# Kernel tuning notes

Measured on AMD Instinct MI355X. Metric: run time of the kernel, lower is better.

The kernel has to match this reference:

```python
import jax, jax.numpy as jnp
import numpy as np

D = 1024
KERNEL = 4

def setup_inputs() -> dict:
    key = jax.random.key(0)
    ks = jax.random.split(key, 8)
    B, L, d = 4, 8192, D
    x = jax.random.normal(ks[0], (B, L, d), dtype=jnp.float32)
    conv_weight = jax.random.normal(ks[1], (d, 1, KERNEL), dtype=jnp.float32) * 0.02
    conv_bias = jnp.zeros((d,), dtype=jnp.float32)
    lim = 1.0 / np.sqrt(d)
    Wr_w = jax.random.uniform(ks[2], (d, d), jnp.float32, -lim, lim)
    Wr_b = jax.random.uniform(ks[3], (d,), jnp.float32, -lim, lim)
    Wi_w = jax.random.uniform(ks[4], (d, d), jnp.float32, -lim, lim)
    Wi_b = jax.random.uniform(ks[5], (d,), jnp.float32, -lim, lim)
    log_a = jnp.full((d,), 7.5, dtype=jnp.float32)
    out_w = jax.random.uniform(ks[6], (d, d), jnp.float32, -lim, lim)
    norm_w = jnp.ones((d,), dtype=jnp.float32)
    return {"x": x, "conv_weight": conv_weight, "conv_bias": conv_bias,
            "Wr_w": Wr_w, "Wr_b": Wr_b, "Wi_w": Wi_w, "Wi_b": Wi_b,
            "log_a": log_a, "out_w": out_w, "norm_w": norm_w}

def _causal_depthwise_conv(x, w, b):
    # x: [B,L,d], w: [d,1,K], b: [d]. out[t] = sum_k w[:,0,k] * x[t-3+k] + b
    B, L, d = x.shape
    xp = jnp.pad(x, ((0, 0), (KERNEL - 1, 0), (0, 0)))
    out = b[None, None, :]
    for k in range(KERNEL):  # small fixed kernel loop
        out = out + xp[:, k:k + L, :] * w[:, 0, k][None, None, :]
    return out

def _parallel_scan(a_t, b_t):
    # h_t = a_t * h_{t-1} + b_t via log-space cumsum; float32 throughout
    a = a_t.astype(jnp.float32)
    b = b_t.astype(jnp.float32)
    log_A = jnp.clip(jnp.cumsum(jnp.log(jnp.clip(a, 1e-7)), axis=1), -80.0, None)
    A = jnp.exp(log_A)
    h = A * jnp.cumsum(b * jnp.exp(-log_A), axis=1)
    return h.astype(a_t.dtype)

def _rmsnorm(x, w, eps=1e-6):
    ms = jnp.mean(jnp.square(x.astype(jnp.float32)), axis=-1, keepdims=True)
    return (x * jax.lax.rsqrt(ms + eps)).astype(x.dtype) * w

def reference(x, conv_weight, conv_bias, Wr_w, Wr_b, Wi_w, Wi_b, log_a, out_w, norm_w):
    x_conv = _causal_depthwise_conv(x, conv_weight, conv_bias)          # [B,L,d]
    r_t = jax.nn.sigmoid(x_conv @ Wr_w.T + Wr_b)
    i_t = jax.nn.sigmoid(x_conv @ Wi_w.T + Wi_b)
    a_base = jax.nn.sigmoid(log_a.astype(jnp.float32)).astype(x.dtype)
    a_t = jnp.power(a_base[None, None, :], 8.0 * r_t)
    b_t = jnp.sqrt(jnp.clip(1.0 - a_t * a_t, 1e-6, None)) * (i_t * x_conv)
    h = _parallel_scan(a_t, b_t)
    return _rmsnorm(h @ out_w.T, norm_w)
```

## Files before the change

### kernel.cpp

```cpp
#include <hip/hip_runtime.h>
#include <hip/hip_bf16.h>

#define D 1024
#define KW 4
#define SEQL 8192
#define BATCH 4
#define MROWS (BATCH*SEQL)
#define SEG 128
#define NSEG (SEQL/SEG)

using bf16 = __hip_bfloat16;
typedef __attribute__((ext_vector_type(8))) short bf16x8_t;
typedef __attribute__((ext_vector_type(4))) float f32x4_t;

__device__ __forceinline__ float sigmoid_f(float x){ return 1.0f/(1.0f + __expf(-x)); }

__device__ __forceinline__ void gload_lds16(const bf16* g, bf16* l){
  __builtin_amdgcn_global_load_lds(
    (const __attribute__((address_space(1))) unsigned int*)g,
    (__attribute__((address_space(3))) unsigned int*)l,
    16, 0, 0);
}

__device__ __forceinline__ void bf16x2_unpack(unsigned int u, float& lo, float& hi){
  union { unsigned int i; float f; } a, b;
  a.i = (u & 0xffffu) << 16;
  b.i = u & 0xffff0000u;
  lo = a.f; hi = b.f;
}
__device__ __forceinline__ unsigned int bf16x2_pack(float lo, float hi){
  unsigned short l = __builtin_bit_cast(unsigned short, __float2bfloat16(lo));
  unsigned short h = __builtin_bit_cast(unsigned short, __float2bfloat16(hi));
  return (unsigned int)l | ((unsigned int)h << 16);
}

__global__ __launch_bounds__(256) void prep_k(const float* __restrict__ Wr, const float* __restrict__ Wi,
                                              const float* __restrict__ Wrb, const float* __restrict__ Wib,
                                              const float* __restrict__ Wo,
                                              bf16* __restrict__ W1, bf16* __restrict__ Wob,
                                              float* __restrict__ b1){
  int idx = blockIdx.x*256 + threadIdx.x;
  if (idx < 2*D*D){
    int n = idx >> 10;
    float v = (n < D) ? Wr[idx] : Wi[idx - D*D];
    W1[idx] = __float2bfloat16(v);
  } else if (idx < 3*D*D){
    int j = idx - 2*D*D;
    Wob[j] = __float2bfloat16(Wo[j]);
  }
  if (idx < 2*D){
    b1[idx] = (idx < D) ? Wrb[idx] : Wib[idx - D];
  }
}

__global__ __launch_bounds__(256) void conv_k(const float* __restrict__ x, const float* __restrict__ w,
                                              const float* __restrict__ bias,
                                              unsigned int* __restrict__ xcb){
  int idx = blockIdx.x*256 + threadIdx.x;
  int c2 = idx & 511;
  int c  = c2 * 2;
  int m  = idx >> 9;
  int l  = m & (SEQL-1);
  const float* wp = w + c*KW;
  float2 b2 = *(const float2*)(bias + c);
  const float* xm = x + (size_t)m*D + c;
  float2 v3 = *(const float2*)xm;
  float2 v2 = (l>=1)? *(const float2*)(xm - D)   : make_float2(0.f,0.f);
  float2 v1 = (l>=2)? *(const float2*)(xm - 2*D) : make_float2(0.f,0.f);
  float2 v0 = (l>=3)? *(const float2*)(xm - 3*D) : make_float2(0.f,0.f);
  float a0 = b2.x + wp[0]*v0.x + wp[1]*v1.x + wp[2]*v2.x + wp[3]*v3.x;
  float a1 = b2.y + wp[4]*v0.y + wp[5]*v1.y + wp[6]*v2.y + wp[7]*v3.y;
  xcb[idx] = bf16x2_pack(a0, a1);
}

template<typename OutT> __device__ __forceinline__ void store_cvt(OutT* p, float v);
template<> __device__ __forceinline__ void store_cvt<float>(float* p, float v){ *p = v; }
template<> __device__ __forceinline__ void store_cvt<bf16>(bf16* p, float v){ *p = __float2bfloat16(v); }

#define MFMA_BF16(a,b,c) __builtin_amdgcn_mfma_f32_16x16x32_bf16((a),(b),(c),0,0,0)

#define GPHASE(buf, q, STAGE_STMT, WAIT_STMT) do{                         \
    bf16x8_t a0 = rdA(buf, 2*(q),   0);                                   \
    bf16x8_t a1 = rdA(buf, 2*(q),   1);                                   \
    bf16x8_t a2 = rdA(buf, 2*(q)+1, 0);                                   \
    bf16x8_t a3 = rdA(buf, 2*(q)+1, 1);                                   \
    if ((q) == 0){                                                        \
      b00 = rdB(buf,0,0); b01 = rdB(buf,0,1);                             \
      b10 = rdB(buf,1,0); b11 = rdB(buf,1,1);                             \
      b20 = rdB(buf,2,0); b21 = rdB(buf,2,1);                             \
      b30 = rdB(buf,3,0); b31 = rdB(buf,3,1);                             \
    }                                                                     \
    STAGE_STMT;                                                           \
    WAIT_STMT;                                                            \
    __builtin_amdgcn_s_barrier();                                         \
    asm volatile("s_waitcnt lgkmcnt(0)" ::: "memory");                    \
    __builtin_amdgcn_s_setprio(1);                                        \
    acc[2*(q)  ][0] = MFMA_BF16(a0, b00, acc[2*(q)  ][0]);                \
    acc[2*(q)  ][0] = MFMA_BF16(a1, b01, acc[2*(q)  ][0]);                \
    acc[2*(q)  ][1] = MFMA_BF16(a0, b10, acc[2*(q)  ][1]);                \
    acc[2*(q)  ][1] = MFMA_BF16(a1, b11, acc[2*(q)  ][1]);                \
    acc[2*(q)  ][2] = MFMA_BF16(a0, b20, acc[2*(q)  ][2]);                \
    acc[2*(q)  ][2] = MFMA_BF16(a1, b21, acc[2*(q)  ][2]);                \
    acc[2*(q)  ][3] = MFMA_BF16(a0, b30, acc[2*(q)  ][3]);                \
    acc[2*(q)  ][3] = MFMA_BF16(a1, b31, acc[2*(q)  ][3]);                \
    acc[2*(q)+1][0] = MFMA_BF16(a2, b00, acc[2*(q)+1][0]);                \
    acc[2*(q)+1][0] = MFMA_BF16(a3, b01, acc[2*(q)+1][0]);                \
    acc[2*(q)+1][1] = MFMA_BF16(a2, b10, acc[2*(q)+1][1]);                \
    acc[2*(q)+1][1] = MFMA_BF16(a3, b11, acc[2*(q)+1][1]);                \
    acc[2*(q)+1][2] = MFMA_BF16(a2, b20, acc[2*(q)+1][2]);                \
    acc[2*(q)+1][2] = MFMA_BF16(a3, b21, acc[2*(q)+1][2]);                \
    acc[2*(q)+1][3] = MFMA_BF16(a2, b30, acc[2*(q)+1][3]);                \
    acc[2*(q)+1][3] = MFMA_BF16(a3, b31, acc[2*(q)+1][3]);                \
    __builtin_amdgcn_s_setprio(0);                                        \
    __builtin_amdgcn_s_barrier();                                         \
}while(0)

#define WAIT_STEADY do{ if (it + 1 < nIter) asm volatile("s_waitcnt vmcnt(4)" ::: "memory"); \
                        else                asm volatile("s_waitcnt vmcnt(0)" ::: "memory"); }while(0)

template<typename OutT, bool HB>
__global__ __launch_bounds__(512, 2) void gemm256(const bf16* __restrict__ A, const bf16* __restrict__ B,
                                                  const float* __restrict__ bias, OutT* __restrict__ C,
                                                  int M, int N, int K){
  __shared__ alignas(128) bf16 Asm[2][256*64];
  __shared__ alignas(128) bf16 Bsm[2][256*64];
  const int t    = threadIdx.x;
  const int wave = t >> 6, lane = t & 63;
  const int wm   = wave >> 2, wn = wave & 3;
  const int lrow = lane & 15, quad = lane >> 4;

  const int nbn = N >> 8;
  const int cpx = gridDim.x >> 3;
  const int bid = blockIdx.x;
  const int swz = (bid & 7) * cpx + (bid >> 3);
  const int m0  = (swz / nbn) << 8;
  const int n0  = (swz % nbn) << 8;

  const int srow = wave*8 + (lane >> 3);
  const int scol = (((lane & 7) ^ (srow & 7)) << 3);

  auto stageA = [&](int tile, int half, int buf){
    const bf16* g = A + (size_t)(m0 + half*128 + srow)*K + tile*64 + scol;
    bf16* l = &Asm[buf][half*128*64 + wave*8*64];
    gload_lds16(g, l);
    gload_lds16(g + (size_t)64*K, l + 64*64);
  };
  auto stageB = [&](int tile, int half, int buf){
    const bf16* g = B + (size_t)(n0 + half*128 + srow)*K + tile*64 + scol;
    bf16* l = &Bsm[buf][half*128*64 + wave*8*64];
    gload_lds16(g, l);
    gload_lds16(g + (size_t)64*K, l + 64*64);
  };
  auto rdA = [&](int buf, int fi, int ks)->bf16x8_t{
    return *(const bf16x8_t*)&Asm[buf][(wm*128 + fi*16 + lrow)*64 + ((((ks)*4 + quad) ^ (lrow & 7)) << 3)];
  };
  auto rdB = [&](int buf, int j, int ks)->bf16x8_t{
    return *(const bf16x8_t*)&Bsm[buf][(wn*64 + j*16 + lrow)*64 + ((((ks)*4 + quad) ^ (lrow & 7)) << 3)];
  };

  f32x4_t acc[8][4];
  #pragma unroll
  for (int i=0;i<8;i++)
    #pragma unroll
    for (int j=0;j<4;j++) acc[i][j] = (f32x4_t){0.f,0.f,0.f,0.f};
  bf16x8_t b00,b01,b10,b11,b20,b21,b30,b31;

  const int nt    = K >> 6;
  const int nIter = nt >> 1;

  stageB(0, 0, 0); stageB(0, 1, 0);
  stageA(0, 0, 0); stageA(0, 1, 0);
  stageB(1, 0, 1); stageB(1, 1, 1);
  asm volatile("s_waitcnt vmcnt(4)" ::: "memory");
  __builtin_amdgcn_s_barrier();

  for (int it = 0; it < nIter; ++it){
    const int t1 = 2*it + 1, t2 = 2*it + 2, t3 = 2*it + 3;
    const bool ok2 = (t2 < nt), ok3 = (t3 < nt);
    GPHASE(0, 0, stageA(t1, 0, 1), );
    GPHASE(0, 1, stageA(t1, 1, 1), );
    GPHASE(0, 2, if (ok2) stageB(t2, 0, 0), );
    GPHASE(0, 3, if (ok2) stageB(t2, 1, 0), WAIT_STEADY);
    GPHASE(1, 0, if (ok2) stageA(t2, 0, 0), );
    GPHASE(1, 1, if (ok2) stageA(t2, 1, 0), );
    GPHASE(1, 2, if (ok3) stageB(t3, 0, 1), );
    GPHASE(1, 3, if (ok3) stageB(t3, 1, 1), WAIT_STEADY);
  }

  #pragma unroll
  for (int i=0;i<8;i++){
    #pragma unroll
    for (int j=0;j<4;j++){
      int gm0 = m0 + wm*128 + i*16 + quad*4;
      int gn  = n0 + wn*64  + j*16 + lrow;
      float bv = HB ? bias[gn] : 0.f;
      #pragma unroll
      for (int r=0;r<4;r++){
        store_cvt(&C[(size_t)(gm0 + r)*N + gn], acc[i][j][r] + bv);
      }
    }
  }
}

__global__ __launch_bounds__(256) void scan1_k(const unsigned int* __restrict__ ri,
                                               const unsigned int* __restrict__ xcb,
                                               const float* __restrict__ log_a,
                                               float* __restrict__ Aprod, float* __restrict__ Hend){
  int idx = blockIdx.x*256 + threadIdx.x;
  int c2 = idx & 511;
  int c  = c2*2;
  int bs = idx >> 9;
  int s  = bs & (NSEG-1);
  int b  = bs >> 6;
  size_t m0 = (size_t)b*SEQL + (size_t)s*SEG;
  float2 la = *(const float2*)(log_a + c);
  float c1x = -8.f * log1pf(__expf(-la.x));
  float c1y = -8.f * log1pf(__expf(-la.y));
  float Ax=1.f, Ay=1.f, hx=0.f, hy=0.f;
  for (int l=0; l<SEG; l++){
    size_t m = m0 + l;
    float zrx, zry, zix, ziy, xvx, xvy;
    bf16x2_unpack(ri[m*D + c2],        zrx, zry);
    bf16x2_unpack(ri[m*D + 512 + c2],  zix, ziy);
    bf16x2_unpack(xcb[m*512 + c2],     xvx, xvy);
    float ax = __expf(c1x * sigmoid_f(zrx));
    float ay = __expf(c1y * sigmoid_f(zry));
    float btx = sqrtf(fmaxf(1.f - ax*ax, 1e-6f)) * sigmoid_f(zix) * xvx;
    float bty = sqrtf(fmaxf(1.f - ay*ay, 1e-6f)) * sigmoid_f(ziy) * xvy;
    Ax *= ax; Ay *= ay;
    hx = fmaf(ax, hx, btx);
    hy = fmaf(ay, hy, bty);
  }
  *(float2*)(Aprod + 2*idx) = make_float2(Ax, Ay);
  *(float2*)(Hend  + 2*idx) = make_float2(hx, hy);
}

__global__ __launch_bounds__(256) void scan2_k(const float* __restrict__ Aprod, const float* __restrict__ Hend,
                                               float* __restrict__ carry){
  int idx = blockIdx.x*256 + threadIdx.x;
  int c = idx & (D-1);
  int b = idx >> 10;
  float h = 0.f;
  #pragma unroll 8
  for (int s=0; s<NSEG; s++){
    int j = ((b*NSEG + s) << 10) + c;
    carry[j] = h;
    h = fmaf(Aprod[j], h, Hend[j]);
  }
}

__global__ __launch_bounds__(256) void scan3_k(const unsigned int* __restrict__ ri,
                                               const unsigned int* __restrict__ xcb,
                                               const float* __restrict__ log_a, const float* __restrict__ carry,
                                               unsigned int* __restrict__ hbuf){
  int idx = blockIdx.x*256 + threadIdx.x;
  int c2 = idx & 511;
  int c  = c2*2;
  int bs = idx >> 9;
  int s  = bs & (NSEG-1);
  int b  = bs >> 6;
  size_t m0 = (size_t)b*SEQL + (size_t)s*SEG;
  float2 la = *(const float2*)(log_a + c);
  float c1x = -8.f * log1pf(__expf(-la.x));
  float c1y = -8.f * log1pf(__expf(-la.y));
  float2 h2 = *(const float2*)(carry + 2*idx);
  float hx = h2.x, hy = h2.y;
  for (int l=0; l<SEG; l++){
    size_t m = m0 + l;
    float zrx, zry, zix, ziy, xvx, xvy;
    bf16x2_unpack(ri[m*D + c2],       zrx, zry);
    bf16x2_unpack(ri[m*D + 512 + c2], zix, ziy);
    bf16x2_unpack(xcb[m*512 + c2],    xvx, xvy);
    float ax = __expf(c1x * sigmoid_f(zrx));
    float ay = __expf(c1y * sigmoid_f(zry));
    float btx = sqrtf(fmaxf(1.f - ax*ax, 1e-6f)) * sigmoid_f(zix) * xvx;
    float bty = sqrtf(fmaxf(1.f - ay*ay, 1e-6f)) * sigmoid_f(ziy) * xvy;
    hx = fmaf(ax, hx, btx);
    hy = fmaf(ay, hy, bty);
    hbuf[m*512 + c2] = bf16x2_pack(hx, hy);
  }
}

__global__ __launch_bounds__(256) void rms_k(float* __restrict__ y, const float* __restrict__ nw){
  int row = blockIdx.x;
  int t   = threadIdx.x;
  float* yr = y + (size_t)row*D;
  f32x4_t v = *(const f32x4_t*)(yr + t*4);
  float ss = v[0]*v[0] + v[1]*v[1] + v[2]*v[2] + v[3]*v[3];
  #pragma unroll
  for (int off=32; off>0; off>>=1) ss += __shfl_down(ss, off);
  __shared__ float red[4];
  if ((t & 63) == 0) red[t>>6] = ss;
  __syncthreads();
  float tot = red[0] + red[1] + red[2] + red[3];
  float scale = rsqrtf(tot * (1.f/D) + 1e-6f);
  f32x4_t w = *(const f32x4_t*)(nw + t*4);
  f32x4_t o;
  #pragma unroll
  for (int k=0;k<4;k++) o[k] = v[k]*scale*w[k];
  *(f32x4_t*)(yr + t*4) = o;
}

extern "C" void kernel_launch(void* const* d_in, const int* in_sizes, int n_in,
                              void* d_out, int out_size, void* d_ws, size_t ws_size,
                              hipStream_t stream) {
  const float* x     = (const float*)d_in[0];
  const float* convw = (const float*)d_in[1];
  const float* convb = (const float*)d_in[2];
  const float* Wr_w  = (const float*)d_in[3];
  const float* Wr_b  = (const float*)d_in[4];
  const float* Wi_w  = (const float*)d_in[5];
  const float* Wi_b  = (const float*)d_in[6];
  const float* log_a = (const float*)d_in[7];
  const float* out_w = (const float*)d_in[8];
  const float* norm_w= (const float*)d_in[9];

  char* ws = (char*)d_ws;
  size_t off = 0;
  auto alloc = [&](size_t bytes)->char*{ char* p = ws + off; off += (bytes + 255) & ~(size_t)255; return p; };

  bf16*  xcb   = (bf16*) alloc((size_t)MROWS*D*2);
  bf16*  ri    = (bf16*) alloc((size_t)MROWS*2*D*2);
  bf16*  hbuf  = (bf16*) alloc((size_t)MROWS*D*2);
  bf16*  W1    = (bf16*) alloc((size_t)2*D*D*2);
  bf16*  Wob   = (bf16*) alloc((size_t)D*D*2);
  float* b1    = (float*)alloc((size_t)2*D*4);
  float* Aprod = (float*)alloc((size_t)BATCH*NSEG*D*4);
  float* Hend  = (float*)alloc((size_t)BATCH*NSEG*D*4);
  float* carry = (float*)alloc((size_t)BATCH*NSEG*D*4);
  float* y     = (float*)d_out;

  prep_k<<<dim3((3*D*D + 255)/256), dim3(256), 0, stream>>>(Wr_w, Wi_w, Wr_b, Wi_b, out_w, W1, Wob, b1);
  conv_k<<<dim3(MROWS*(D/2)/256), dim3(256), 0, stream>>>(x, convw, convb, (unsigned int*)xcb);
  gemm256<bf16, true><<<dim3((MROWS/256)*((2*D)/256)), dim3(512), 0, stream>>>(xcb, W1, b1, ri, MROWS, 2*D, D);
  scan1_k<<<dim3(BATCH*NSEG*(D/2)/256), dim3(256), 0, stream>>>((const unsigned int*)ri, (const unsigned int*)xcb, log_a, Aprod, Hend);
  scan2_k<<<dim3(BATCH*D/256), dim3(256), 0, stream>>>(Aprod, Hend, carry);
  scan3_k<<<dim3(BATCH*NSEG*(D/2)/256), dim3(256), 0, stream>>>((const unsigned int*)ri, (const unsigned int*)xcb, log_a, carry, (unsigned int*)hbuf);
  gemm256<float, false><<<dim3((MROWS/256)*(D/256)), dim3(512), 0, stream>>>(hbuf, Wob, nullptr, y, MROWS, D, D);
  rms_k<<<dim3(MROWS), dim3(256), 0, stream>>>(y, norm_w);
}
```

Measured before the change: 740.6 us.

## Shorten scan segments, vectorize conv and scans to 4 channels, reuse xcb buffer

Scan segment length drops from 128 to 32, so scan1 and scan3 launch more threads with shorter serial chains. The carry pass in scan2 grows to 256 sequential steps. The conv, scan1 and scan3 kernels now handle four channels per thread with wider 16-byte and 8-byte loads and stores, which cuts instruction overhead and memory transactions. scan3 writes h in place over the xcb buffer instead of a separate hbuf, which removes one workspace allocation and lets the output GEMM read from xcb.

```diff
diff --git a/kernel.cpp b/kernel.cpp
--- a/kernel.cpp
+++ b/kernel.cpp
@@ -6,7 +6,7 @@
 #define SEQL 8192
 #define BATCH 4
 #define MROWS (BATCH*SEQL)
-#define SEG 128
+#define SEG 32
 #define NSEG (SEQL/SEG)
 
 using bf16 = __hip_bfloat16;
@@ -57,20 +57,30 @@
                                               const float* __restrict__ bias,
                                               unsigned int* __restrict__ xcb){
   int idx = blockIdx.x*256 + threadIdx.x;
-  int c2 = idx & 511;
-  int c  = c2 * 2;
-  int m  = idx >> 9;
+  int c4 = idx & 255;
+  int c  = c4 * 4;
+  int m  = idx >> 8;
   int l  = m & (SEQL-1);
   const float* wp = w + c*KW;
-  float2 b2 = *(const float2*)(bias + c);
+  f32x4_t t0 = *(const f32x4_t*)(wp);
+  f32x4_t t1 = *(const f32x4_t*)(wp + 4);
+  f32x4_t t2 = *(const f32x4_t*)(wp + 8);
+  f32x4_t t3 = *(const f32x4_t*)(wp + 12);
+  f32x4_t bb = *(const f32x4_t*)(bias + c);
   const float* xm = x + (size_t)m*D + c;
-  float2 v3 = *(const float2*)xm;
-  float2 v2 = (l>=1)? *(const float2*)(xm - D)   : make_float2(0.f,0.f);
-  float2 v1 = (l>=2)? *(const float2*)(xm - 2*D) : make_float2(0.f,0.f);
-  float2 v0 = (l>=3)? *(const float2*)(xm - 3*D) : make_float2(0.f,0.f);
-  float a0 = b2.x + wp[0]*v0.x + wp[1]*v1.x + wp[2]*v2.x + wp[3]*v3.x;
-  float a1 = b2.y + wp[4]*v0.y + wp[5]*v1.y + wp[6]*v2.y + wp[7]*v3.y;
-  xcb[idx] = bf16x2_pack(a0, a1);
+  f32x4_t v3 = *(const f32x4_t*)xm;
+  f32x4_t z  = (f32x4_t){0.f,0.f,0.f,0.f};
+  f32x4_t v2 = (l>=1)? *(const f32x4_t*)(xm - D)   : z;
+  f32x4_t v1 = (l>=2)? *(const f32x4_t*)(xm - 2*D) : z;
+  f32x4_t v0 = (l>=3)? *(const f32x4_t*)(xm - 3*D) : z;
+  float a0 = bb[0] + t0[0]*v0[0] + t0[1]*v1[0] + t0[2]*v2[0] + t0[3]*v3[0];
+  float a1 = bb[1] + t1[0]*v0[1] + t1[1]*v1[1] + t1[2]*v2[1] + t1[3]*v3[1];
+  float a2 = bb[2] + t2[0]*v0[2] + t2[1]*v1[2] + t2[2]*v2[2] + t2[3]*v3[2];
+  float a3 = bb[3] + t3[0]*v0[3] + t3[1]*v1[3] + t3[2]*v2[3] + t3[3]*v3[3];
+  uint2 o;
+  o.x = bf16x2_pack(a0, a1);
+  o.y = bf16x2_pack(a2, a3);
+  *(uint2*)(xcb + (size_t)m*512 + 2*c4) = o;
 }
 
 template<typename OutT> __device__ __forceinline__ void store_cvt(OutT* p, float v);
@@ -207,32 +217,38 @@
                                                const float* __restrict__ log_a,
                                                float* __restrict__ Aprod, float* __restrict__ Hend){
   int idx = blockIdx.x*256 + threadIdx.x;
-  int c2 = idx & 511;
-  int c  = c2*2;
-  int bs = idx >> 9;
+  int c4 = idx & 255;
+  int c  = c4*4;
+  int bs = idx >> 8;
   int s  = bs & (NSEG-1);
-  int b  = bs >> 6;
+  int b  = bs >> 8;
   size_t m0 = (size_t)b*SEQL + (size_t)s*SEG;
-  float2 la = *(const float2*)(log_a + c);
-  float c1x = -8.f * log1pf(__expf(-la.x));
-  float c1y = -8.f * log1pf(__expf(-la.y));
-  float Ax=1.f, Ay=1.f, hx=0.f, hy=0.f;
+  f32x4_t la = *(const f32x4_t*)(log_a + c);
+  float c1[4];
+  #pragma unroll
+  for (int j=0;j<4;j++) c1[j] = -8.f * log1pf(__expf(-la[j]));
+  float A[4] = {1.f,1.f,1.f,1.f};
+  float h[4] = {0.f,0.f,0.f,0.f};
+  #pragma unroll 4
   for (int l=0; l<SEG; l++){
     size_t m = m0 + l;
-    float zrx, zry, zix, ziy, xvx, xvy;
-    bf16x2_unpack(ri[m*D + c2],        zrx, zry);
-    bf16x2_unpack(ri[m*D + 512 + c2],  zix, ziy);
-    bf16x2_unpack(xcb[m*512 + c2],     xvx, xvy);
-    float ax = __expf(c1x * sigmoid_f(zrx));
-    float ay = __expf(c1y * sigmoid_f(zry));
-    float btx = sqrtf(fmaxf(1.f - ax*ax, 1e-6f)) * sigmoid_f(zix) * xvx;
-    float bty = sqrtf(fmaxf(1.f - ay*ay, 1e-6f)) * sigmoid_f(ziy) * xvy;
-    Ax *= ax; Ay *= ay;
-    hx = fmaf(ax, hx, btx);
-    hy = fmaf(ay, hy, bty);
-  }
-  *(float2*)(Aprod + 2*idx) = make_float2(Ax, Ay);
-  *(float2*)(Hend  + 2*idx) = make_float2(hx, hy);
+    uint2 uzr = *(const uint2*)(ri  + m*1024 + 2*c4);
+    uint2 uzi = *(const uint2*)(ri  + m*1024 + 512 + 2*c4);
+    uint2 uxv = *(const uint2*)(xcb + m*512  + 2*c4);
+    float zr[4], zi[4], xv[4];
+    bf16x2_unpack(uzr.x, zr[0], zr[1]); bf16x2_unpack(uzr.y, zr[2], zr[3]);
+    bf16x2_unpack(uzi.x, zi[0], zi[1]); bf16x2_unpack(uzi.y, zi[2], zi[3]);
+    bf16x2_unpack(uxv.x, xv[0], xv[1]); bf16x2_unpack(uxv.y, xv[2], xv[3]);
+    #pragma unroll
+    for (int j=0;j<4;j++){
+      float a  = __expf(c1[j] * sigmoid_f(zr[j]));
+      float bt = sqrtf(fmaxf(1.f - a*a, 1e-6f)) * sigmoid_f(zi[j]) * xv[j];
+      A[j] *= a;
+      h[j]  = fmaf(a, h[j], bt);
+    }
+  }
+  *(f32x4_t*)(Aprod + 4*(size_t)idx) = (f32x4_t){A[0],A[1],A[2],A[3]};
+  *(f32x4_t*)(Hend  + 4*(size_t)idx) = (f32x4_t){h[0],h[1],h[2],h[3]};
 }
 
 __global__ __launch_bounds__(256) void scan2_k(const float* __restrict__ Aprod, const float* __restrict__ Hend,
@@ -244,40 +260,49 @@
   #pragma unroll 8
   for (int s=0; s<NSEG; s++){
     int j = ((b*NSEG + s) << 10) + c;
+    float a = Aprod[j];
+    float e = Hend[j];
     carry[j] = h;
-    h = fmaf(Aprod[j], h, Hend[j]);
+    h = fmaf(a, h, e);
   }
 }
 
 __global__ __launch_bounds__(256) void scan3_k(const unsigned int* __restrict__ ri,
-                                               const unsigned int* __restrict__ xcb,
-                                               const float* __restrict__ log_a, const float* __restrict__ carry,
-                                               unsigned int* __restrict__ hbuf){
-  int idx = blockIdx.x*256 + threadIdx.x;
-  int c2 = idx & 511;
-  int c  = c2*2;
-  int bs = idx >> 9;
+                                               unsigned int* xcb,
+                                               const float* __restrict__ log_a, const float* __restrict__ carry){
+  int idx = blockIdx.x*256 + threadIdx.x;
+  int c4 = idx & 255;
+  int c  = c4*4;
+  int bs = idx >> 8;
   int s  = bs & (NSEG-1);
-  int b  = bs >> 6;
+  int b  = bs >> 8;
   size_t m0 = (size_t)b*SEQL + (size_t)s*SEG;
-  float2 la = *(const float2*)(log_a + c);
-  float c1x = -8.f * log1pf(__expf(-la.x));
-  float c1y = -8.f * log1pf(__expf(-la.y));
-  float2 h2 = *(const float2*)(carry + 2*idx);
-  float hx = h2.x, hy = h2.y;
+  f32x4_t la = *(const f32x4_t*)(log_a + c);
+  float c1[4];
+  #pragma unroll
+  for (int j=0;j<4;j++) c1[j] = -8.f * log1pf(__expf(-la[j]));
+  f32x4_t h4 = *(const f32x4_t*)(carry + 4*(size_t)idx);
+  float h[4] = {h4[0], h4[1], h4[2], h4[3]};
+  #pragma unroll 4
   for (int l=0; l<SEG; l++){
     size_t m = m0 + l;
-    float zrx, zry, zix, ziy, xvx, xvy;
-    bf16x2_unpack(ri[m*D + c2],       zrx, zry);
-    bf16x2_unpack(ri[m*D + 512 + c2], zix, ziy);
-    bf16x2_unpack(xcb[m*512 + c2],    xvx, xvy);
-    float ax = __expf(c1x * sigmoid_f(zrx));
-    float ay = __expf(c1y * sigmoid_f(zry));
-    float btx = sqrtf(fmaxf(1.f - ax*ax, 1e-6f)) * sigmoid_f(zix) * xvx;
-    float bty = sqrtf(fmaxf(1.f - ay*ay, 1e-6f)) * sigmoid_f(ziy) * xvy;
-    hx = fmaf(ax, hx, btx);
-    hy = fmaf(ay, hy, bty);
-    hbuf[m*512 + c2] = bf16x2_pack(hx, hy);
+    uint2 uzr = *(const uint2*)(ri  + m*1024 + 2*c4);
+    uint2 uzi = *(const uint2*)(ri  + m*1024 + 512 + 2*c4);
+    uint2 uxv = *(const uint2*)(xcb + m*512  + 2*c4);
+    float zr[4], zi[4], xv[4];
+    bf16x2_unpack(uzr.x, zr[0], zr[1]); bf16x2_unpack(uzr.y, zr[2], zr[3]);
+    bf16x2_unpack(uzi.x, zi[0], zi[1]); bf16x2_unpack(uzi.y, zi[2], zi[3]);
+    bf16x2_unpack(uxv.x, xv[0], xv[1]); bf16x2_unpack(uxv.y, xv[2], xv[3]);
+    #pragma unroll
+    for (int j=0;j<4;j++){
+      float a  = __expf(c1[j] * sigmoid_f(zr[j]));
+      float bt = sqrtf(fmaxf(1.f - a*a, 1e-6f)) * sigmoid_f(zi[j]) * xv[j];
+      h[j] = fmaf(a, h[j], bt);
+    }
+    uint2 o;
+    o.x = bf16x2_pack(h[0], h[1]);
+    o.y = bf16x2_pack(h[2], h[3]);
+    *(uint2*)(xcb + m*512 + 2*c4) = o;
   }
 }
 
@@ -321,7 +346,6 @@
 
   bf16*  xcb   = (bf16*) alloc((size_t)MROWS*D*2);
   bf16*  ri    = (bf16*) alloc((size_t)MROWS*2*D*2);
-  bf16*  hbuf  = (bf16*) alloc((size_t)MROWS*D*2);
   bf16*  W1    = (bf16*) alloc((size_t)2*D*D*2);
   bf16*  Wob   = (bf16*) alloc((size_t)D*D*2);
   float* b1    = (float*)alloc((size_t)2*D*4);
@@ -331,11 +355,11 @@
   float* y     = (float*)d_out;
 
   prep_k<<<dim3((3*D*D + 255)/256), dim3(256), 0, stream>>>(Wr_w, Wi_w, Wr_b, Wi_b, out_w, W1, Wob, b1);
-  conv_k<<<dim3(MROWS*(D/2)/256), dim3(256), 0, stream>>>(x, convw, convb, (unsigned int*)xcb);
+  conv_k<<<dim3(MROWS*(D/4)/256), dim3(256), 0, stream>>>(x, convw, convb, (unsigned int*)xcb);
   gemm256<bf16, true><<<dim3((MROWS/256)*((2*D)/256)), dim3(512), 0, stream>>>(xcb, W1, b1, ri, MROWS, 2*D, D);
-  scan1_k<<<dim3(BATCH*NSEG*(D/2)/256), dim3(256), 0, stream>>>((const unsigned int*)ri, (const unsigned int*)xcb, log_a, Aprod, Hend);
+  scan1_k<<<dim3(BATCH*NSEG*(D/4)/256), dim3(256), 0, stream>>>((const unsigned int*)ri, (const unsigned int*)xcb, log_a, Aprod, Hend);
   scan2_k<<<dim3(BATCH*D/256), dim3(256), 0, stream>>>(Aprod, Hend, carry);
-  scan3_k<<<dim3(BATCH*NSEG*(D/2)/256), dim3(256), 0, stream>>>((const unsigned int*)ri, (const unsigned int*)xcb, log_a, carry, (unsigned int*)hbuf);
-  gemm256<float, false><<<dim3((MROWS/256)*(D/256)), dim3(512), 0, stream>>>(hbuf, Wob, nullptr, y, MROWS, D, D);
+  scan3_k<<<dim3(BATCH*NSEG*(D/4)/256), dim3(256), 0, stream>>>((const unsigned int*)ri, (unsigned int*)xcb, log_a, carry);
+  gemm256<float, false><<<dim3((MROWS/256)*(D/256)), dim3(512), 0, stream>>>(xcb, Wob, nullptr, y, MROWS, D, D);
   rms_k<<<dim3(MROWS), dim3(256), 0, stream>>>(y, norm_w);
 }
```

Result: faster. 696.1 us (-6.0%).
